# Performance work log

Hardware: AMD Instinct MI355X
Metric: run time of the kernel (lower is better)

The kernel has to match this reference:

```python
import jax, jax.numpy as jnp
import numpy as np

H, FFN, E, TOPK = 1024, 4096, 8, 2
B, S = 2, 1024


def setup_inputs() -> dict:
    key = jax.random.key(0)
    k1, k2, k3, k4 = jax.random.split(key, 4)
    s_h = 1.0 / np.sqrt(H).astype(np.float32)
    s_f = 1.0 / np.sqrt(FFN).astype(np.float32)
    return {
        "hidden_states": jax.random.normal(k1, (B, S, H), jnp.float32),
        "gate_w": jax.random.normal(k2, (E, H), jnp.float32) * s_h,       # router Linear(H->E), no bias
        "w13": jax.random.normal(k3, (E, 2 * FFN, H), jnp.float32) * s_h,  # fused [w1; w3] per expert
        "w2": jax.random.normal(k4, (E, H, FFN), jnp.float32) * s_f,       # down-proj per expert
        "top_k": TOPK,
    }


def reference(hidden_states, gate_w, w13, w2, top_k):
    b, s, h = hidden_states.shape
    x = hidden_states.reshape(-1, h)                       # [T, H]
    router_logits = x @ gate_w.T                           # [T, E]
    rw = jax.nn.softmax(router_logits.astype(jnp.float32), axis=1)
    rw, sel = jax.lax.top_k(rw, top_k)                     # [T, K] each
    rw = rw / rw.sum(axis=-1, keepdims=True)
    rw = rw.astype(x.dtype)
    e_tot = gate_w.shape[0]
    f = w2.shape[2]
    # combine[t, e] = sum_k rw[t, k] * (sel[t, k] == e)
    combine = jnp.sum((sel[..., None] == jnp.arange(e_tot)) * rw[..., None], axis=1)  # [T, E]
    out = jnp.zeros_like(x)
    for e in range(e_tot):  # static small loop over experts
        g = x @ w13[e, :f].T            # [T, F] gate proj
        u = x @ w13[e, f:].T            # [T, F] up proj
        y = (jax.nn.silu(g) * u) @ w2[e].T  # [T, H]
        out = out + combine[:, e:e + 1] * y
    return out.reshape(b, s, h), router_logits
```

## Files before the change

### kernel.cpp

```cpp
#include <hip/hip_runtime.h>
#include <math.h>

#define H     1024
#define FFN   4096
#define NE    8
#define TOK   2048
#define PAIRS (TOK*2)
#define BM    128
#define BK    32
#define ROWCAP (PAIRS + NE*BM)
#define MAXTILES (ROWCAP/BM)

typedef unsigned short u16;
typedef __attribute__((ext_vector_type(8))) __bf16 bf16x8;
typedef __attribute__((ext_vector_type(4))) float  f32x4;

struct alignas(8) us4 { u16 x, y, z, w; };

__device__ __forceinline__ u16 f2bf(float f) {
    unsigned u = __builtin_bit_cast(unsigned, f);
    return (u16)((u + 0x7fffu + ((u >> 16) & 1u)) >> 16);
}

#define GLD16(gp, lp) __builtin_amdgcn_global_load_lds( \
    (const __attribute__((address_space(1))) void*)(gp), \
    (__attribute__((address_space(3))) void*)(lp), 16, 0, 0)

__global__ void k_zero(int* counts, uint4* xg4) {
    size_t i = (size_t)blockIdx.x * 256 + threadIdx.x;
    if (i < (size_t)ROWCAP * H / 8) xg4[i] = uint4{0u, 0u, 0u, 0u};
    if (blockIdx.x == 0 && threadIdx.x < NE) counts[threadIdx.x] = 0;
}

__global__ void k_router(const float* __restrict__ x, const float* __restrict__ gw,
                         float* __restrict__ logits, int* counts,
                         int* __restrict__ sel, int* __restrict__ posn, float* __restrict__ wgt) {
    int lane = threadIdx.x & 63;
    int t = blockIdx.x * 4 + (threadIdx.x >> 6);
    float p[NE];
#pragma unroll
    for (int e = 0; e < NE; e++) p[e] = 0.f;
    for (int j = 0; j < H / 64; j++) {
        int h = lane + j * 64;
        float xv = x[(size_t)t * H + h];
#pragma unroll
        for (int e = 0; e < NE; e++) p[e] = fmaf(xv, gw[e * H + h], p[e]);
    }
#pragma unroll
    for (int off = 32; off; off >>= 1)
#pragma unroll
        for (int e = 0; e < NE; e++) p[e] += __shfl_xor(p[e], off, 64);
    if (lane == 0) {
        float mx = p[0];
#pragma unroll
        for (int e = 1; e < NE; e++) mx = fmaxf(mx, p[e]);
        float pe[NE];
#pragma unroll
        for (int e = 0; e < NE; e++) pe[e] = __expf(p[e] - mx);
        int i0 = 0;
#pragma unroll
        for (int e = 1; e < NE; e++) if (pe[e] > pe[i0]) i0 = e;
        int i1 = (i0 == 0) ? 1 : 0;
#pragma unroll
        for (int e = 0; e < NE; e++) if (e != i1 && e != i0 && pe[e] > pe[i1]) i1 = e;
        float w0 = pe[i0] / (pe[i0] + pe[i1]);
#pragma unroll
        for (int e = 0; e < NE; e++) logits[(size_t)t * NE + e] = p[e];
        int p0 = atomicAdd(&counts[i0], 1);
        int p1 = atomicAdd(&counts[i1], 1);
        sel[2 * t] = i0;  posn[2 * t] = p0;  wgt[2 * t] = w0;
        sel[2 * t + 1] = i1;  posn[2 * t + 1] = p1;  wgt[2 * t + 1] = 1.f - w0;
    }
}

__global__ void k_prefix(const int* __restrict__ counts, int* __restrict__ base,
                         int* __restrict__ tile_e) {
    if (threadIdx.x == 0) {
        int b = 0, tb = 0;
        for (int e = 0; e < NE; e++) {
            base[e] = b;
            int nt = (counts[e] + BM - 1) / BM;
            for (int i = 0; i < nt; i++) tile_e[tb++] = e;
            b += nt * BM;
        }
        base[NE] = b;
        while (tb < MAXTILES) tile_e[tb++] = -1;
    }
}

__global__ void k_gather(const float4* __restrict__ x4, const int* __restrict__ sel,
                         const int* __restrict__ posn, const int* __restrict__ base,
                         u16* __restrict__ xg) {
    int p = blockIdx.x;
    int lane = threadIdx.x;
    int t = p >> 1;
    int row = base[sel[p]] + posn[p];
#pragma unroll
    for (int i = 0; i < 4; i++) {
        int idx = i * 64 + lane;
        float4 v = x4[(size_t)t * (H / 4) + idx];
        us4 o = { f2bf(v.x), f2bf(v.y), f2bf(v.z), f2bf(v.w) };
        *(us4*)&xg[(size_t)row * H + idx * 4] = o;
    }
}

__global__ __launch_bounds__(256) void k_gemm1(const u16* __restrict__ xg,
                                               const float* __restrict__ w13,
                                               u16* __restrict__ act,
                                               const int* __restrict__ tile_e) {
    int e = tile_e[blockIdx.x];
    if (e < 0) return;
    __shared__ u16 As[BM * BK];
    __shared__ u16 Bs[2][64 * (BK + 8)];

    int tid = threadIdx.x;
    int lane = tid & 63, wave = tid >> 6;
    int quad = lane >> 4, m16 = lane & 15;
    int wm = wave >> 1, wn = wave & 1;
    int row0 = blockIdx.x * BM;
    int n0 = blockIdx.y * 64;
    const float* wb1 = w13 + ((size_t)e * 2 * FFN + n0) * H;
    const float* wb3 = w13 + ((size_t)e * 2 * FFN + FFN + n0) * H;

    f32x4 accg[4][2], accu[4][2];
#pragma unroll
    for (int mi = 0; mi < 4; mi++)
#pragma unroll
        for (int ni = 0; ni < 2; ni++) { accg[mi][ni] = {0.f,0.f,0.f,0.f}; accu[mi][ni] = {0.f,0.f,0.f,0.f}; }

    for (int kk = 0; kk < H; kk += BK) {
#pragma unroll
        for (int i = 0; i < 2; i++) {
            int chunk = i * 256 + tid;
            int r = chunk >> 2, c = (chunk & 3) * 8;
            GLD16(xg + (size_t)(row0 + r) * H + kk + c, As + chunk * 8);
        }
#pragma unroll
        for (int i = 0; i < 2; i++) {
            int idx = i * 256 + tid;
            int r = idx >> 3, c4 = idx & 7;
            float4 v1 = *(const float4*)(wb1 + (size_t)r * H + kk + c4 * 4);
            float4 v3 = *(const float4*)(wb3 + (size_t)r * H + kk + c4 * 4);
            us4 o1 = { f2bf(v1.x), f2bf(v1.y), f2bf(v1.z), f2bf(v1.w) };
            us4 o3 = { f2bf(v3.x), f2bf(v3.y), f2bf(v3.z), f2bf(v3.w) };
            *(us4*)&Bs[0][r * (BK + 8) + c4 * 4] = o1;
            *(us4*)&Bs[1][r * (BK + 8) + c4 * 4] = o3;
        }
        __syncthreads();
        bf16x8 a[4], bg[2], bu[2];
#pragma unroll
        for (int mi = 0; mi < 4; mi++)
            a[mi] = *(const bf16x8*)&As[(wm * 64 + mi * 16 + m16) * BK + quad * 8];
#pragma unroll
        for (int ni = 0; ni < 2; ni++) {
            bg[ni] = *(const bf16x8*)&Bs[0][(wn * 32 + ni * 16 + m16) * (BK + 8) + quad * 8];
            bu[ni] = *(const bf16x8*)&Bs[1][(wn * 32 + ni * 16 + m16) * (BK + 8) + quad * 8];
        }
#pragma unroll
        for (int mi = 0; mi < 4; mi++)
#pragma unroll
            for (int ni = 0; ni < 2; ni++) {
                accg[mi][ni] = __builtin_amdgcn_mfma_f32_16x16x32_bf16(a[mi], bg[ni], accg[mi][ni], 0, 0, 0);
                accu[mi][ni] = __builtin_amdgcn_mfma_f32_16x16x32_bf16(a[mi], bu[ni], accu[mi][ni], 0, 0, 0);
            }
        __syncthreads();
    }
#pragma unroll
    for (int mi = 0; mi < 4; mi++)
#pragma unroll
        for (int ni = 0; ni < 2; ni++)
#pragma unroll
            for (int r = 0; r < 4; r++) {
                float g = accg[mi][ni][r], u = accu[mi][ni][r];
                float hv = g * (1.f / (1.f + __expf(-g))) * u;
                int grow = row0 + wm * 64 + mi * 16 + quad * 4 + r;
                int gcol = n0 + wn * 32 + ni * 16 + m16;
                act[(size_t)grow * FFN + gcol] = f2bf(hv);
            }
}

__global__ __launch_bounds__(256) void k_gemm2(const u16* __restrict__ act,
                                               const float* __restrict__ w2,
                                               float* __restrict__ yc,
                                               const int* __restrict__ tile_e) {
    int e = tile_e[blockIdx.x];
    if (e < 0) return;
    __shared__ u16 As[BM * BK];
    __shared__ u16 Bs[BM * (BK + 8)];

    int tid = threadIdx.x;
    int lane = tid & 63, wave = tid >> 6;
    int quad = lane >> 4, m16 = lane & 15;
    int wm = wave >> 1, wn = wave & 1;
    int row0 = blockIdx.x * BM;
    int n0 = blockIdx.y * 128;
    const float* wb = w2 + ((size_t)e * H + n0) * FFN;

    f32x4 acc[4][4];
#pragma unroll
    for (int mi = 0; mi < 4; mi++)
#pragma unroll
        for (int ni = 0; ni < 4; ni++) acc[mi][ni] = {0.f,0.f,0.f,0.f};

    for (int kk = 0; kk < FFN; kk += BK) {
#pragma unroll
        for (int i = 0; i < 2; i++) {
            int chunk = i * 256 + tid;
            int r = chunk >> 2, c = (chunk & 3) * 8;
            GLD16(act + (size_t)(row0 + r) * FFN + kk + c, As + chunk * 8);
        }
#pragma unroll
        for (int i = 0; i < 4; i++) {
            int idx = i * 256 + tid;
            int r = idx >> 3, c4 = idx & 7;
            float4 v = *(const float4*)(wb + (size_t)r * FFN + kk + c4 * 4);
            us4 o = { f2bf(v.x), f2bf(v.y), f2bf(v.z), f2bf(v.w) };
            *(us4*)&Bs[r * (BK + 8) + c4 * 4] = o;
        }
        __syncthreads();
        bf16x8 a[4], b[4];
#pragma unroll
        for (int mi = 0; mi < 4; mi++)
            a[mi] = *(const bf16x8*)&As[(wm * 64 + mi * 16 + m16) * BK + quad * 8];
#pragma unroll
        for (int ni = 0; ni < 4; ni++)
            b[ni] = *(const bf16x8*)&Bs[(wn * 64 + ni * 16 + m16) * (BK + 8) + quad * 8];
#pragma unroll
        for (int mi = 0; mi < 4; mi++)
#pragma unroll
            for (int ni = 0; ni < 4; ni++)
                acc[mi][ni] = __builtin_amdgcn_mfma_f32_16x16x32_bf16(a[mi], b[ni], acc[mi][ni], 0, 0, 0);
        __syncthreads();
    }
#pragma unroll
    for (int mi = 0; mi < 4; mi++)
#pragma unroll
        for (int ni = 0; ni < 4; ni++)
#pragma unroll
            for (int r = 0; r < 4; r++) {
                int grow = row0 + wm * 64 + mi * 16 + quad * 4 + r;
                int gcol = n0 + wn * 64 + ni * 16 + m16;
                yc[(size_t)grow * H + gcol] = acc[mi][ni][r];
            }
}

__global__ void k_combine(const float4* __restrict__ yc4, const int* __restrict__ sel,
                          const int* __restrict__ posn, const int* __restrict__ base,
                          const float* __restrict__ wgt, float4* __restrict__ out4) {
    int t = blockIdx.x;
    int j = threadIdx.x;
    int r0 = base[sel[2 * t]] + posn[2 * t];
    int r1 = base[sel[2 * t + 1]] + posn[2 * t + 1];
    float w0 = wgt[2 * t], w1 = wgt[2 * t + 1];
    float4 a = yc4[(size_t)r0 * (H / 4) + j];
    float4 b = yc4[(size_t)r1 * (H / 4) + j];
    float4 o = { w0 * a.x + w1 * b.x, w0 * a.y + w1 * b.y,
                 w0 * a.z + w1 * b.z, w0 * a.w + w1 * b.w };
    out4[(size_t)t * (H / 4) + j] = o;
}

extern "C" void kernel_launch(void* const* d_in, const int* in_sizes, int n_in,
                              void* d_out, int out_size, void* d_ws, size_t ws_size,
                              hipStream_t stream) {
    const float* x   = (const float*)d_in[0];
    const float* gw  = (const float*)d_in[1];
    const float* w13 = (const float*)d_in[2];
    const float* w2  = (const float*)d_in[3];
    float* out    = (float*)d_out;
    float* logits = out + (size_t)TOK * H;

    char* ws = (char*)d_ws;
    int*   counts = (int*)ws;
    int*   base   = (int*)(ws + 256);
    int*   tile_e = (int*)(ws + 512);
    int*   sel    = (int*)(ws + 1024);
    int*   posn   = (int*)(ws + 1024 + 4 * PAIRS);
    float* wgt    = (float*)(ws + 1024 + 8 * PAIRS);
    u16*   xg     = (u16*)(ws + 65536);
    u16*   act    = xg + (size_t)ROWCAP * H;
    float* yc     = (float*)(act + (size_t)ROWCAP * FFN);

    k_zero<<<2560, 256, 0, stream>>>(counts, (uint4*)xg);
    k_router<<<TOK / 4, 256, 0, stream>>>(x, gw, logits, counts, sel, posn, wgt);
    k_prefix<<<1, 64, 0, stream>>>(counts, base, tile_e);
    k_gather<<<PAIRS, 64, 0, stream>>>((const float4*)x, sel, posn, base, xg);
    dim3 g1(MAXTILES, FFN / 64);
    k_gemm1<<<g1, 256, 0, stream>>>(xg, w13, act, tile_e);
    dim3 g2(MAXTILES, H / 128);
    k_gemm2<<<g2, 256, 0, stream>>>(act, w2, yc, tile_e);
    k_combine<<<TOK, 256, 0, stream>>>((const float4*)yc, sel, posn, base, wgt, (float4*)out);
}
```

Measured before the change: 771.7 us.

## Split gemm2 along K into two partial buffers, drop xg zeroing, use packed bf16 conversion

Splits the down-projection GEMM along FFN into two halves over grid z, each writing its own partial yc buffer, and the combine kernel sums the two partials. This doubles the block count of gemm2, which otherwise has few blocks, to raise occupancy. It also removes the full zeroing of the gathered activation buffer, leaving padding rows with garbage that only feeds rows the combine never reads. The bf16 conversions now use the packed hardware intrinsic. The cost is twice the yc buffer size and extra reads in combine.

```diff
diff --git a/kernel.cpp b/kernel.cpp
--- a/kernel.cpp
+++ b/kernel.cpp
@@ -1,4 +1,5 @@
 #include <hip/hip_runtime.h>
+#include <hip/hip_bf16.h>
 #include <math.h>
 
 #define H     1024
@@ -15,21 +16,19 @@
 typedef __attribute__((ext_vector_type(8))) __bf16 bf16x8;
 typedef __attribute__((ext_vector_type(4))) float  f32x4;
 
-struct alignas(8) us4 { u16 x, y, z, w; };
-
-__device__ __forceinline__ u16 f2bf(float f) {
-    unsigned u = __builtin_bit_cast(unsigned, f);
-    return (u16)((u + 0x7fffu + ((u >> 16) & 1u)) >> 16);
+__device__ __forceinline__ unsigned cvt2(float a, float b) {
+    __hip_bfloat162 h = __float22bfloat162_rn(float2{a, b});
+    unsigned u;
+    __builtin_memcpy(&u, &h, 4);
+    return u;
 }
 
 #define GLD16(gp, lp) __builtin_amdgcn_global_load_lds( \
     (const __attribute__((address_space(1))) void*)(gp), \
     (__attribute__((address_space(3))) void*)(lp), 16, 0, 0)
 
-__global__ void k_zero(int* counts, uint4* xg4) {
-    size_t i = (size_t)blockIdx.x * 256 + threadIdx.x;
-    if (i < (size_t)ROWCAP * H / 8) xg4[i] = uint4{0u, 0u, 0u, 0u};
-    if (blockIdx.x == 0 && threadIdx.x < NE) counts[threadIdx.x] = 0;
+__global__ void k_init(int* counts) {
+    if (threadIdx.x < NE) counts[threadIdx.x] = 0;
 }
 
 __global__ void k_router(const float* __restrict__ x, const float* __restrict__ gw,
@@ -99,8 +98,8 @@
     for (int i = 0; i < 4; i++) {
         int idx = i * 64 + lane;
         float4 v = x4[(size_t)t * (H / 4) + idx];
-        us4 o = { f2bf(v.x), f2bf(v.y), f2bf(v.z), f2bf(v.w) };
-        *(us4*)&xg[(size_t)row * H + idx * 4] = o;
+        uint2 o = { cvt2(v.x, v.y), cvt2(v.z, v.w) };
+        *(uint2*)&xg[(size_t)row * H + idx * 4] = o;
     }
 }
 
@@ -141,10 +140,10 @@
             int r = idx >> 3, c4 = idx & 7;
             float4 v1 = *(const float4*)(wb1 + (size_t)r * H + kk + c4 * 4);
             float4 v3 = *(const float4*)(wb3 + (size_t)r * H + kk + c4 * 4);
-            us4 o1 = { f2bf(v1.x), f2bf(v1.y), f2bf(v1.z), f2bf(v1.w) };
-            us4 o3 = { f2bf(v3.x), f2bf(v3.y), f2bf(v3.z), f2bf(v3.w) };
-            *(us4*)&Bs[0][r * (BK + 8) + c4 * 4] = o1;
-            *(us4*)&Bs[1][r * (BK + 8) + c4 * 4] = o3;
+            uint2 o1 = { cvt2(v1.x, v1.y), cvt2(v1.z, v1.w) };
+            uint2 o3 = { cvt2(v3.x, v3.y), cvt2(v3.z, v3.w) };
+            *(uint2*)&Bs[0][r * (BK + 8) + c4 * 4] = o1;
+            *(uint2*)&Bs[1][r * (BK + 8) + c4 * 4] = o3;
         }
         __syncthreads();
         bf16x8 a[4], bg[2], bu[2];
@@ -168,15 +167,17 @@
 #pragma unroll
     for (int mi = 0; mi < 4; mi++)
 #pragma unroll
-        for (int ni = 0; ni < 2; ni++)
+        for (int ni = 0; ni < 2; ni++) {
+            int gcol = n0 + wn * 32 + ni * 16 + m16;
+            int grow = row0 + wm * 64 + mi * 16 + quad * 4;
 #pragma unroll
             for (int r = 0; r < 4; r++) {
                 float g = accg[mi][ni][r], u = accu[mi][ni][r];
                 float hv = g * (1.f / (1.f + __expf(-g))) * u;
-                int grow = row0 + wm * 64 + mi * 16 + quad * 4 + r;
-                int gcol = n0 + wn * 32 + ni * 16 + m16;
-                act[(size_t)grow * FFN + gcol] = f2bf(hv);
+                unsigned pk = cvt2(hv, hv);
+                act[(size_t)(grow + r) * FFN + gcol] = (u16)(pk & 0xffff);
             }
+        }
 }
 
 __global__ __launch_bounds__(256) void k_gemm2(const u16* __restrict__ act,
@@ -194,7 +195,9 @@
     int wm = wave >> 1, wn = wave & 1;
     int row0 = blockIdx.x * BM;
     int n0 = blockIdx.y * 128;
+    int k0 = blockIdx.z * (FFN / 2);
     const float* wb = w2 + ((size_t)e * H + n0) * FFN;
+    float* ycp = yc + (size_t)blockIdx.z * ROWCAP * H;
 
     f32x4 acc[4][4];
 #pragma unroll
@@ -202,7 +205,7 @@
 #pragma unroll
         for (int ni = 0; ni < 4; ni++) acc[mi][ni] = {0.f,0.f,0.f,0.f};
 
-    for (int kk = 0; kk < FFN; kk += BK) {
+    for (int kk = k0; kk < k0 + FFN / 2; kk += BK) {
 #pragma unroll
         for (int i = 0; i < 2; i++) {
             int chunk = i * 256 + tid;
@@ -214,8 +217,8 @@
             int idx = i * 256 + tid;
             int r = idx >> 3, c4 = idx & 7;
             float4 v = *(const float4*)(wb + (size_t)r * FFN + kk + c4 * 4);
-            us4 o = { f2bf(v.x), f2bf(v.y), f2bf(v.z), f2bf(v.w) };
-            *(us4*)&Bs[r * (BK + 8) + c4 * 4] = o;
+            uint2 o = { cvt2(v.x, v.y), cvt2(v.z, v.w) };
+            *(uint2*)&Bs[r * (BK + 8) + c4 * 4] = o;
         }
         __syncthreads();
         bf16x8 a[4], b[4];
@@ -240,7 +243,7 @@
             for (int r = 0; r < 4; r++) {
                 int grow = row0 + wm * 64 + mi * 16 + quad * 4 + r;
                 int gcol = n0 + wn * 64 + ni * 16 + m16;
-                yc[(size_t)grow * H + gcol] = acc[mi][ni][r];
+                ycp[(size_t)grow * H + gcol] = acc[mi][ni][r];
             }
 }
 
@@ -252,10 +255,15 @@
     int r0 = base[sel[2 * t]] + posn[2 * t];
     int r1 = base[sel[2 * t + 1]] + posn[2 * t + 1];
     float w0 = wgt[2 * t], w1 = wgt[2 * t + 1];
-    float4 a = yc4[(size_t)r0 * (H / 4) + j];
-    float4 b = yc4[(size_t)r1 * (H / 4) + j];
-    float4 o = { w0 * a.x + w1 * b.x, w0 * a.y + w1 * b.y,
-                 w0 * a.z + w1 * b.z, w0 * a.w + w1 * b.w };
+    const size_t P = (size_t)ROWCAP * (H / 4);
+    float4 a0 = yc4[(size_t)r0 * (H / 4) + j];
+    float4 a1 = yc4[(size_t)r0 * (H / 4) + j + P];
+    float4 b0 = yc4[(size_t)r1 * (H / 4) + j];
+    float4 b1 = yc4[(size_t)r1 * (H / 4) + j + P];
+    float4 o = { w0 * (a0.x + a1.x) + w1 * (b0.x + b1.x),
+                 w0 * (a0.y + a1.y) + w1 * (b0.y + b1.y),
+                 w0 * (a0.z + a1.z) + w1 * (b0.z + b1.z),
+                 w0 * (a0.w + a1.w) + w1 * (b0.w + b1.w) };
     out4[(size_t)t * (H / 4) + j] = o;
 }
 
@@ -280,13 +288,13 @@
     u16*   act    = xg + (size_t)ROWCAP * H;
     float* yc     = (float*)(act + (size_t)ROWCAP * FFN);
 
-    k_zero<<<2560, 256, 0, stream>>>(counts, (uint4*)xg);
+    k_init<<<1, 64, 0, stream>>>(counts);
     k_router<<<TOK / 4, 256, 0, stream>>>(x, gw, logits, counts, sel, posn, wgt);
     k_prefix<<<1, 64, 0, stream>>>(counts, base, tile_e);
     k_gather<<<PAIRS, 64, 0, stream>>>((const float4*)x, sel, posn, base, xg);
     dim3 g1(MAXTILES, FFN / 64);
     k_gemm1<<<g1, 256, 0, stream>>>(xg, w13, act, tile_e);
-    dim3 g2(MAXTILES, H / 128);
+    dim3 g2(MAXTILES, H / 128, 2);
     k_gemm2<<<g2, 256, 0, stream>>>(act, w2, yc, tile_e);
     k_combine<<<TOK, 256, 0, stream>>>((const float4*)yc, sel, posn, base, wgt, (float4*)out);
 }
```

After: 720.0 us. 1.07x faster.
